# Kernel optimization log

Measured on AMD Instinct MI355X. Metric: run time of the kernel, lower is better.

The kernel has to match this reference:

```python
import jax, jax.numpy as jnp
import numpy as np

N = 64  # periodic element grid per side; nnode = N^3, ndof = 3*N^3
OFFSETS = [(0,0,0),(1,0,0),(0,1,0),(1,1,0),(0,0,1),(1,0,1),(0,1,1),(1,1,1)]


def setup_inputs() -> dict:
    key = jax.random.key(0)
    k1, k2, k3 = jax.random.split(key, 3)
    ndof = 3 * N ** 3
    U = jax.random.normal(k1, (ndof,), jnp.float32)
    rho = jax.random.uniform(k2, (N, N, N), jnp.float32)
    # nodIdx [nel, 8]: the 8 corner nodes of each element with periodic wrap
    idx = np.arange(N)
    I, J, K = np.meshgrid(idx, idx, idx, indexing='ij')
    cols = []
    for (di, dj, dk) in OFFSETS:
        n = (((I + di) % N) * N + (J + dj) % N) * N + (K + dk) % N
        cols.append(n.reshape(-1))
    nodIdx = jnp.asarray(np.stack(cols, axis=1), jnp.int32)  # [nel, 8]
    # 256 element stiffness matrices (24x24, symmetric), one per H8 type code
    filters = jax.random.normal(k3, (256, 24, 24), jnp.float32) * 0.05
    filters = 0.5 * (filters + filters.transpose(0, 2, 1))
    # typeFilter: 2x2x2 powers-of-two kernel encoding corner occupancy pattern
    typeFilter = jnp.asarray((2.0 ** np.arange(8)).reshape(2, 2, 2), jnp.float32)
    return {"U": U, "rho": rho, "nodIdx": nodIdx, "filters": filters, "typeFilter": typeFilter}


def _typeH8(rho, typeFilter):
    # binarize density and compute per-element type code via periodic 2x2x2 conv
    rb = (rho > 0.5).astype(rho.dtype)
    t = jnp.zeros_like(rho)
    for (di, dj, dk) in OFFSETS:
        t = t + typeFilter[di, dj, dk] * jnp.roll(rb, shift=(-di, -dj, -dk), axis=(0, 1, 2))
    return jax.lax.stop_gradient(t).astype(jnp.int32).reshape(-1)  # [nel] in 0..255


def reference(U, rho, nodIdx, filters, typeFilter):
    types = _typeH8(rho, typeFilter)                       # [nel]
    # dof indices per element: 8 nodes x 3 dofs, periodic wrap baked into nodIdx
    dofIdx = (nodIdx.astype(jnp.int32)[:, :, None] * 3 + jnp.arange(3, dtype=jnp.int32)).reshape(-1, 24)
    Ue = U[dofIdx]                                         # [nel, 24] gather
    Ke = filters[types]                                    # [nel, 24, 24] type-conditional filter select
    KUe = jnp.einsum('eij,ej->ei', Ke, Ue)                 # element-local stiffness apply
    KU = jnp.zeros_like(U).at[dofIdx.reshape(-1)].add(KUe.reshape(-1))  # scatter-add assembly
    return KU
```

## Files before the change

kernel.cpp:

```cpp
#include <hip/hip_runtime.h>
#include <hip/hip_fp16.h>

#define NGRID 64
#define NEL (NGRID*NGRID*NGRID)
#define IDX(i,j,k) ((((i)*64 + (j)) * 64) + (k))

#define NSLAB    16
#define SLAB_EL  16384
#define NTYPE    256
#define NCHUNK   16
#define CAP      32

#define RHO_EL   2176
#define STAGE_EL 1152
#define K5_LDS   (8*STAGE_EL*8)

#define WS_U4     0
#define WS_KUE    (WS_U4 + (size_t)NEL*8)
#define WS_SORTED (WS_KUE + (size_t)NEL*64)
#define WS_CNT    (WS_SORTED + (size_t)256*NTYPE*CAP*4)
#define WS_NEEDED (size_t)(WS_CNT + NSLAB*NTYPE*NCHUNK*4)

__device__ __forceinline__ int type_of(const float* __restrict__ rho, int i, int j, int k) {
    int i1 = (i + 1) & 63, j1 = (j + 1) & 63, k1 = (k + 1) & 63;
    int t = 0;
    t |= (rho[IDX(i,  j,  k )] > 0.5f ? 1 : 0) << 0;
    t |= (rho[IDX(i1, j,  k )] > 0.5f ? 1 : 0) << 4;
    t |= (rho[IDX(i,  j1, k )] > 0.5f ? 1 : 0) << 2;
    t |= (rho[IDX(i1, j1, k )] > 0.5f ? 1 : 0) << 6;
    t |= (rho[IDX(i,  j,  k1)] > 0.5f ? 1 : 0) << 1;
    t |= (rho[IDX(i1, j,  k1)] > 0.5f ? 1 : 0) << 5;
    t |= (rho[IDX(i,  j1, k1)] > 0.5f ? 1 : 0) << 3;
    t |= (rho[IDX(i1, j1, k1)] > 0.5f ? 1 : 0) << 7;
    return t;
}

__global__ __launch_bounds__(1024) void k1_pack_scatter(
    const float* __restrict__ U, const float* __restrict__ rho,
    uint2* __restrict__ U4h, int* __restrict__ sorted, int* __restrict__ cntmat)
{
    __shared__ int lh[NTYPE];
    __shared__ int rb[RHO_EL];
    __shared__ float us[3072];
    int tid = threadIdx.x;
    int b = blockIdx.x;
    int slab = b & 15, chunk = b >> 4;
    int i  = slab * 4 + (chunk >> 2);
    int j0 = (chunk & 3) << 4;
    if (tid < NTYPE) lh[tid] = 0;

    int base = slab * SLAB_EL + chunk * 1024;
    if (tid < 768)
        ((float4*)us)[tid] = ((const float4*)(U + (size_t)base * 3))[tid];

    for (int f = tid; f < RHO_EL; f += 1024) {
        int pi = (f >= 1088) ? 1 : 0;
        int rem = f - pi * 1088;
        int pj = rem >> 6, kk = rem & 63;
        int ei = (i + pi) & 63;
        int ej = (j0 + pj) & 63;
        rb[f] = rho[IDX(ei, ej, kk)] > 0.5f ? 1 : 0;
    }
    __syncthreads();

    int e = base + tid;
    union { __half2 h; unsigned u; } pxy, pz;
    pxy.h = __floats2half2_rn(us[3*tid + 0], us[3*tid + 1]);
    pz.h  = __floats2half2_rn(us[3*tid + 2], 0.0f);
    U4h[e] = make_uint2(pxy.u, pz.u);

    int k = tid & 63, jj = tid >> 6;
    int t = 0;
    #pragma unroll
    for (int di = 0; di < 2; ++di)
        #pragma unroll
        for (int dj = 0; dj < 2; ++dj)
            #pragma unroll
            for (int dk = 0; dk < 2; ++dk)
                t |= rb[di*1088 + (jj + dj)*64 + ((k + dk) & 63)] << (di*4 + dj*2 + dk);

    int rank = atomicAdd(&lh[t], 1);
    if (rank < CAP)
        sorted[((slab * NCHUNK + chunk) * NTYPE + t) * CAP + rank] = e;
    __syncthreads();
    if (tid < NTYPE)
        cntmat[(slab * NTYPE + tid) * NCHUNK + chunk] = lh[tid];
}

__global__ __launch_bounds__(256) void k4_apply(
    const uint2* __restrict__ U4h, const float* __restrict__ filters,
    const int* __restrict__ sorted, const int* __restrict__ cntmat,
    float4* __restrict__ KUe16)
{
    int b = blockIdx.x;
    int slab = (b & 7) + 8 * (b >> 10);
    int q    = (b >> 3) & 127;
    int w    = threadIdx.x >> 6;
    int tt   = __builtin_amdgcn_readfirstlane(2 * q + (w >> 1));
    int h    = (w & 1);

    const int4* crow = (const int4*)(cntmat + (slab * NTYPE + tt) * NCHUNK);
    int4 c0 = crow[0], c1 = crow[1], c2 = crow[2], c3 = crow[3];
    int c[16] = { c0.x,c0.y,c0.z,c0.w, c1.x,c1.y,c1.z,c1.w,
                  c2.x,c2.y,c2.z,c2.w, c3.x,c3.y,c3.z,c3.w };
    int total = 0;
    #pragma unroll
    for (int f = 0; f < 16; ++f) total += c[f];
    total = __builtin_amdgcn_readfirstlane(total);
    if (total <= h * 64) return;

    int g = h * 64 + (threadIdx.x & 63);
    const float* __restrict__ F = filters + tt * 576;

    if (g < total) {
        int acc = 0, frag = 0, off = 0;
        bool found = false;
        #pragma unroll
        for (int f = 0; f < 16; ++f) {
            int nacc = acc + c[f];
            bool hit = (!found) && (g < nacc);
            frag = hit ? f : frag;
            off  = hit ? g - acc : off;
            found = found || hit;
            acc = nacc;
        }
        int e = sorted[((slab * NCHUNK + frag) * NTYPE + tt) * CAP + off];
        e &= (NEL - 1);

        int k = e & 63, j = (e >> 6) & 63, i = (e >> 12) & 63;
        int i1 = (i + 1) & 63, j1 = (j + 1) & 63, k1 = (k + 1) & 63;
        int nodes[8];
        nodes[0] = IDX(i,  j,  k );
        nodes[1] = IDX(i1, j,  k );
        nodes[2] = IDX(i,  j1, k );
        nodes[3] = IDX(i1, j1, k );
        nodes[4] = IDX(i,  j,  k1);
        nodes[5] = IDX(i1, j,  k1);
        nodes[6] = IDX(i,  j1, k1);
        nodes[7] = IDX(i1, j1, k1);
        float Ue[24];
        #pragma unroll
        for (int m = 0; m < 8; ++m) {
            uint2 u = U4h[nodes[m]];
            union { unsigned v; __half2 h2; } ux, uz;
            ux.v = u.x; uz.v = u.y;
            Ue[3*m + 0] = __low2float(ux.h2);
            Ue[3*m + 1] = __high2float(ux.h2);
            Ue[3*m + 2] = __low2float(uz.h2);
        }
        float o[24];
        #pragma unroll
        for (int r = 0; r < 24; ++r) {
            float a = 0.0f;
            #pragma unroll
            for (int qq = 0; qq < 24; ++qq)
                a = fmaf(F[r * 24 + qq], Ue[qq], a);
            o[r] = a;
        }
        union { __half2 hh[16]; float4 ff[4]; } ob;
        #pragma unroll
        for (int cc = 0; cc < 8; ++cc) {
            ob.hh[2*cc + 0] = __floats2half2_rn(o[3*cc + 0], o[3*cc + 1]);
            ob.hh[2*cc + 1] = __floats2half2_rn(o[3*cc + 2], 0.0f);
        }
        float4* __restrict__ dst = KUe16 + (size_t)e * 4;
        #pragma unroll
        for (int qq = 0; qq < 4; ++qq) dst[qq] = ob.ff[qq];
    }
}

__global__ __launch_bounds__(512) void k5_reduce(
    const uint4* __restrict__ KUe4, float* __restrict__ out)
{
    extern __shared__ uint2 cache[];
    int tid = threadIdx.x;
    int b = blockIdx.x;
    int hi = b >> 3;
    int slab  = (b & 7) + 8 * (hi >> 5);
    int inner = hi & 31;
    int i  = slab * 4 + (inner >> 3);
    int j0 = (inner & 7) << 3;
    int im1 = (i - 1) & 63;

    for (int f = tid; f < STAGE_EL * 4; f += 512) {
        int le = f >> 2, s = f & 3;
        int pi = (le >= 576) ? 1 : 0;
        int rem = le - pi * 576;
        int pj = rem >> 6, ek = rem & 63;
        int ei = pi ? i : im1;
        int ej = (j0 - 1 + pj) & 63;
        uint4 v = KUe4[(size_t)IDX(ei, ej, ek) * 4 + s];
        cache[(2*s)     * STAGE_EL + le] = make_uint2(v.x, v.y);
        cache[(2*s + 1) * STAGE_EL + le] = make_uint2(v.z, v.w);
    }
    __syncthreads();

    int jj = tid >> 6, k = tid & 63;
    const int DI[8] = {0,1,0,1,0,1,0,1};
    const int DJ[8] = {0,0,1,1,0,0,1,1};
    const int DK[8] = {0,0,0,0,1,1,1,1};
    float a0 = 0.f, a1 = 0.f, a2 = 0.f;
    #pragma unroll
    for (int c = 0; c < 8; ++c) {
        int pi = 1 - DI[c];
        int pj = jj + 1 - DJ[c];
        int ek = (k - DK[c]) & 63;
        uint2 v = cache[c * STAGE_EL + pi * 576 + pj * 64 + ek];
        union { unsigned u; __half2 h; } ux, uy;
        ux.u = v.x; uy.u = v.y;
        a0 += __low2float(ux.h);
        a1 += __high2float(ux.h);
        a2 += __low2float(uy.h);
    }

    float* fs = (float*)cache;
    __syncthreads();
    fs[3*tid + 0] = a0;
    fs[3*tid + 1] = a1;
    fs[3*tid + 2] = a2;
    __syncthreads();
    int n0 = i * 4096 + j0 * 64;
    float4* __restrict__ o4 = (float4*)(out + (size_t)n0 * 3);
    if (tid < 384) o4[tid] = ((float4*)fs)[tid];
}

__global__ __launch_bounds__(256) void fe_apply_atomic(
    const float* __restrict__ U, const float* __restrict__ rho,
    const float* __restrict__ filters, float* __restrict__ out)
{
    int e = blockIdx.x * blockDim.x + threadIdx.x;
    int k = e & 63, j = (e >> 6) & 63, i = (e >> 12) & 63;
    int i1 = (i + 1) & 63, j1 = (j + 1) & 63, k1 = (k + 1) & 63;
    int nodes[8];
    nodes[0]=IDX(i,j,k);   nodes[1]=IDX(i1,j,k);   nodes[2]=IDX(i,j1,k);   nodes[3]=IDX(i1,j1,k);
    nodes[4]=IDX(i,j,k1);  nodes[5]=IDX(i1,j,k1);  nodes[6]=IDX(i,j1,k1);  nodes[7]=IDX(i1,j1,k1);
    int t = type_of(rho, i, j, k);
    float Ue[24];
    #pragma unroll
    for (int m = 0; m < 8; ++m) {
        int bb = nodes[m] * 3;
        Ue[3*m+0]=U[bb+0]; Ue[3*m+1]=U[bb+1]; Ue[3*m+2]=U[bb+2];
    }
    const float4* Kr = (const float4*)(filters + t * 576);
    #pragma unroll
    for (int r = 0; r < 24; ++r) {
        float a = 0.f;
        #pragma unroll
        for (int q = 0; q < 6; ++q) {
            float4 f = Kr[r*6+q];
            a = fmaf(f.x,Ue[4*q+0],a); a = fmaf(f.y,Ue[4*q+1],a);
            a = fmaf(f.z,Ue[4*q+2],a); a = fmaf(f.w,Ue[4*q+3],a);
        }
        atomicAdd(&out[nodes[r/3]*3 + (r%3)], a);
    }
}

extern "C" void kernel_launch(void* const* d_in, const int* in_sizes, int n_in,
                              void* d_out, int out_size, void* d_ws, size_t ws_size,
                              hipStream_t stream) {
    const float* U       = (const float*)d_in[0];
    const float* rho     = (const float*)d_in[1];
    const float* filters = (const float*)d_in[3];
    float* out = (float*)d_out;

    if (ws_size < WS_NEEDED) {
        hipMemsetAsync(out, 0, (size_t)out_size * sizeof(float), stream);
        fe_apply_atomic<<<dim3(NEL/256), dim3(256), 0, stream>>>(U, rho, filters, out);
        return;
    }

    char* ws = (char*)d_ws;
    uint2*  U4h    = (uint2*)(ws + WS_U4);
    float4* KUe16  = (float4*)(ws + WS_KUE);
    int*    sorted = (int*)(ws + WS_SORTED);
    int*    cntmat = (int*)(ws + WS_CNT);

    (void)hipFuncSetAttribute((const void*)k5_reduce,
                              hipFuncAttributeMaxDynamicSharedMemorySize, K5_LDS);

    k1_pack_scatter<<<dim3(256),  dim3(1024), 0,      stream>>>(U, rho, U4h, sorted, cntmat);
    k4_apply       <<<dim3(2048), dim3(256),  0,      stream>>>(U4h, filters, sorted, cntmat, KUe16);
    k5_reduce      <<<dim3(512),  dim3(512),  K5_LDS, stream>>>((const uint4*)KUe16, out);
}
```

Baseline: 35.38 us.

## Enlarge gather-reduce tile to 4x8x32 with halo and restructure element matvec loop

The nodal reduce kernel now handles a 4x8x32 block of nodes per 1024-thread workgroup, staging a 5x9x33 halo of element contributions in LDS. The old 1x8x64 tile re-read a full neighbouring i-plane per block, so this cuts the halo re-read overhead on global memory. In exchange it needs more LDS per block, has fewer blocks (256), and uses integer divisions in the staging loop. Separately, the element matvec now computes three rows per node group and packs them to half straight away, which shortens the live range of the output array.

```diff
diff --git a/kernel.cpp b/kernel.cpp
--- a/kernel.cpp
+++ b/kernel.cpp
@@ -12,8 +12,9 @@
 #define CAP      32
 
 #define RHO_EL   2176
-#define STAGE_EL 1152
-#define K5_LDS   (8*STAGE_EL*8)
+
+#define SE       1485
+#define K5_LDS   (SE*64)
 
 #define WS_U4     0
 #define WS_KUE    (WS_U4 + (size_t)NEL*8)
@@ -148,20 +149,18 @@
             Ue[3*m + 1] = __high2float(ux.h2);
             Ue[3*m + 2] = __low2float(uz.h2);
         }
-        float o[24];
-        #pragma unroll
-        for (int r = 0; r < 24; ++r) {
-            float a = 0.0f;
+        union { __half2 hh[16]; float4 ff[4]; } ob;
+        #pragma unroll
+        for (int cc = 0; cc < 8; ++cc) {
+            float r0 = 0.f, r1 = 0.f, r2 = 0.f;
             #pragma unroll
-            for (int qq = 0; qq < 24; ++qq)
-                a = fmaf(F[r * 24 + qq], Ue[qq], a);
-            o[r] = a;
-        }
-        union { __half2 hh[16]; float4 ff[4]; } ob;
-        #pragma unroll
-        for (int cc = 0; cc < 8; ++cc) {
-            ob.hh[2*cc + 0] = __floats2half2_rn(o[3*cc + 0], o[3*cc + 1]);
-            ob.hh[2*cc + 1] = __floats2half2_rn(o[3*cc + 2], 0.0f);
+            for (int qq = 0; qq < 24; ++qq) {
+                r0 = fmaf(F[(3*cc + 0) * 24 + qq], Ue[qq], r0);
+                r1 = fmaf(F[(3*cc + 1) * 24 + qq], Ue[qq], r1);
+                r2 = fmaf(F[(3*cc + 2) * 24 + qq], Ue[qq], r2);
+            }
+            ob.hh[2*cc + 0] = __floats2half2_rn(r0, r1);
+            ob.hh[2*cc + 1] = __floats2half2_rn(r2, 0.0f);
         }
         float4* __restrict__ dst = KUe16 + (size_t)e * 4;
         #pragma unroll
@@ -169,43 +168,44 @@
     }
 }
 
-__global__ __launch_bounds__(512) void k5_reduce(
+__global__ __launch_bounds__(1024) void k5_reduce(
     const uint4* __restrict__ KUe4, float* __restrict__ out)
 {
     extern __shared__ uint2 cache[];
     int tid = threadIdx.x;
     int b = blockIdx.x;
-    int hi = b >> 3;
-    int slab  = (b & 7) + 8 * (hi >> 5);
-    int inner = hi & 31;
-    int i  = slab * 4 + (inner >> 3);
+    int slab  = (b & 7) + 8 * (b >> 7);
+    int inner = (b >> 3) & 15;
+    int i0 = slab * 4;
     int j0 = (inner & 7) << 3;
-    int im1 = (i - 1) & 63;
-
-    for (int f = tid; f < STAGE_EL * 4; f += 512) {
+    int k0 = (inner >> 3) << 5;
+
+    for (int f = tid; f < SE * 4; f += 1024) {
         int le = f >> 2, s = f & 3;
-        int pi = (le >= 576) ? 1 : 0;
-        int rem = le - pi * 576;
-        int pj = rem >> 6, ek = rem & 63;
-        int ei = pi ? i : im1;
+        int pi = le / 297;
+        int rem = le - pi * 297;
+        int pj = rem / 33;
+        int pe = rem - pj * 33;
+        int ei = (i0 - 1 + pi) & 63;
         int ej = (j0 - 1 + pj) & 63;
+        int ek = (k0 - 1 + pe) & 63;
         uint4 v = KUe4[(size_t)IDX(ei, ej, ek) * 4 + s];
-        cache[(2*s)     * STAGE_EL + le] = make_uint2(v.x, v.y);
-        cache[(2*s + 1) * STAGE_EL + le] = make_uint2(v.z, v.w);
-    }
-    __syncthreads();
-
-    int jj = tid >> 6, k = tid & 63;
+        cache[(2*s)     * SE + le] = make_uint2(v.x, v.y);
+        cache[(2*s + 1) * SE + le] = make_uint2(v.z, v.w);
+    }
+    __syncthreads();
+
+    int ii = tid >> 8, jj = (tid >> 5) & 7, kk = tid & 31;
     const int DI[8] = {0,1,0,1,0,1,0,1};
     const int DJ[8] = {0,0,1,1,0,0,1,1};
     const int DK[8] = {0,0,0,0,1,1,1,1};
     float a0 = 0.f, a1 = 0.f, a2 = 0.f;
     #pragma unroll
     for (int c = 0; c < 8; ++c) {
-        int pi = 1 - DI[c];
+        int pi = ii + 1 - DI[c];
         int pj = jj + 1 - DJ[c];
-        int ek = (k - DK[c]) & 63;
-        uint2 v = cache[c * STAGE_EL + pi * 576 + pj * 64 + ek];
+        int pe = kk + 1 - DK[c];
+        uint2 v = cache[c * SE + pi * 297 + pj * 33 + pe];
         union { unsigned u; __half2 h; } ux, uy;
         ux.u = v.x; uy.u = v.y;
         a0 += __low2float(ux.h);
@@ -219,9 +219,13 @@
     fs[3*tid + 1] = a1;
     fs[3*tid + 2] = a2;
     __syncthreads();
-    int n0 = i * 4096 + j0 * 64;
-    float4* __restrict__ o4 = (float4*)(out + (size_t)n0 * 3);
-    if (tid < 384) o4[tid] = ((float4*)fs)[tid];
+    if (tid < 768) {
+        int r = tid / 24, cq = tid - r * 24;
+        int rii = r >> 3, rjj = r & 7;
+        int n = (i0 + rii) * 4096 + (j0 + rjj) * 64 + k0;
+        float4* __restrict__ o4 = (float4*)(out + (size_t)n * 3);
+        o4[cq] = ((float4*)fs)[r * 24 + cq];
+    }
 }
 
 __global__ __launch_bounds__(256) void fe_apply_atomic(
@@ -280,5 +284,5 @@
 
     k1_pack_scatter<<<dim3(256),  dim3(1024), 0,      stream>>>(U, rho, U4h, sorted, cntmat);
     k4_apply       <<<dim3(2048), dim3(256),  0,      stream>>>(U4h, filters, sorted, cntmat, KUe16);
-    k5_reduce      <<<dim3(512),  dim3(512),  K5_LDS, stream>>>((const uint4*)KUe16, out);
-}
+    k5_reduce      <<<dim3(256),  dim3(1024), K5_LDS, stream>>>((const uint4*)KUe16, out);
+}
```

New measurement: 33.25 us. 1.06x faster.
